# Optimization experiments

Hardware: AMD Instinct MI355X
Metric: run time of the kernel (lower is better)

## Reference

```python
import jax, jax.numpy as jnp
import numpy as np

B, S1, S2, E, P = 8, 2048, 2048, 1024, 1024


def setup_inputs() -> dict:
    key = jax.random.key(0)
    k1, k2, k3, k4, k5 = jax.random.split(key, 5)
    query = jax.random.normal(k1, (B, S1, E), dtype=jnp.float32)
    key_t = jax.random.normal(k2, (B, S2, E), dtype=jnp.float32)
    value = jax.random.normal(k3, (B, S2, E), dtype=jnp.float32)
    # nn.Linear(E, P): weight (P, E), bias (P), shared by q/k/v per the source
    bound = 1.0 / np.sqrt(E)
    W = jax.random.uniform(k4, (P, E), minval=-bound, maxval=bound, dtype=jnp.float32)
    b = jax.random.uniform(k5, (P,), minval=-bound, maxval=bound, dtype=jnp.float32)
    return {"query": query, "key": key_t, "value": value, "W": W, "b": b}


def reference(query, key, value, W, b):
    # Source applies queries_projection to all three inputs.
    q = jnp.einsum("bse,pe->bsp", query, W) + b  # (B,S1,P)
    k = jnp.einsum("bse,pe->bsp", key, W) + b    # (B,S2,P)
    v = jnp.einsum("bse,pe->bsp", value, W) + b  # (B,S2,P)
    scale = 1.0 / jnp.sqrt(jnp.float32(k.shape[-1]))
    scores = jnp.einsum("bqp,bkp->bqk", q, k) * scale  # (B,S1,S2)
    weights = jax.nn.softmax(scores, axis=-1)
    return jnp.einsum("bqk,bkp->bqp", weights, v)  # (B,S1,P)
```

## Files before the change

### kernel.cpp

```cpp
#include <hip/hip_runtime.h>


typedef unsigned short u16;
typedef __bf16 bf16x8 __attribute__((ext_vector_type(8)));
typedef float f32x4 __attribute__((ext_vector_type(4)));

__device__ __forceinline__ float b2f(u16 u) {
    union { unsigned i; float f; } x; x.i = ((unsigned)u) << 16; return x.f;
}
__device__ __forceinline__ u16 f2b(float f) {
    union { float f; unsigned i; } x; x.f = f;
    unsigned r = x.i + 0x7FFFu + ((x.i >> 16) & 1u);
    return (u16)(r >> 16);
}

__global__ __launch_bounds__(256)
void convert_f32_bf16(const float* __restrict__ src, u16* __restrict__ dst, long n)
{
    long i = ((long)blockIdx.x * 256 + threadIdx.x) * 8;
    if (i >= n) return;
    const float4* s = (const float4*)(src + i);
    float4 a = s[0], b = s[1];
    ushort4 lo, hi;
    lo.x = f2b(a.x); lo.y = f2b(a.y); lo.z = f2b(a.z); lo.w = f2b(a.w);
    hi.x = f2b(b.x); hi.y = f2b(b.y); hi.z = f2b(b.z); hi.w = f2b(b.w);
    *(ushort4*)(dst + i) = lo;
    *(ushort4*)(dst + i + 4) = hi;
}


#define BARX()   __builtin_amdgcn_s_barrier()
#define WAITL0() asm volatile("s_waitcnt lgkmcnt(0)" ::: "memory")
#define WV4()    asm volatile("s_waitcnt vmcnt(4)" ::: "memory")
#define WV0()    asm volatile("s_waitcnt vmcnt(0)" ::: "memory")
#define PRIO1()  __builtin_amdgcn_s_setprio(1)
#define PRIO0()  __builtin_amdgcn_s_setprio(0)

__global__ __launch_bounds__(512, 2)
void gemm8(const u16* __restrict__ A, const u16* __restrict__ B,
           void* __restrict__ C, const u16* __restrict__ bias,
           int K, float alpha, int em, int ldc,
           long zA, long zB, long zC, int pw, int ph)
{
    __shared__ __align__(16) u16 lds[65536];

    const int z = blockIdx.z;
    const u16* Ap = A + zA * z;
    const u16* Bp = B + zB * z;
    const long coff = zC * z;

    int tx = blockIdx.x, ty = blockIdx.y;
    if (pw > 0) {
        const int gx = gridDim.x;
        const int lin = ty * gx + tx;
        const int xcd = lin & 7, ii = lin >> 3;
        const int pcols = gx / pw;
        const int pr = xcd / pcols, pc = xcd - pr * pcols;
        tx = pc * pw + (ii % pw);
        ty = pr * ph + (ii / pw);
    }
    const int bm0 = ty << 8, bn0 = tx << 8;

    const int tid = threadIdx.x;
    const int wave = tid >> 6, lane = tid & 63;
    const int wm = wave >> 2, wn = wave & 3;
    const int quad = lane >> 4, l15 = lane & 15;
    const int sw = l15 & 7;

    const int srow = (wave << 3) + (lane >> 3);
    const int sgc  = (((lane & 7) ^ (lane >> 3)) << 3);
    const int sdst = (wave << 9) + (lane << 3);

#define STG_A(b, h, kt) do {                                                          \
    _Pragma("unroll")                                                                 \
    for (int q_ = 0; q_ < 2; ++q_)                                                    \
        __builtin_amdgcn_global_load_lds(                                             \
            (const __attribute__((address_space(1))) void*)(                          \
                Ap + (long)(bm0 + (h)*128 + q_*64 + srow) * K + (kt) + sgc),          \
            (__attribute__((address_space(3))) void*)(                                \
                lds + (b)*32768 + ((h)*128 + q_*64)*64 + sdst),                       \
            16, 0, 0);                                                                \
} while (0)

#define STG_B(b, h, kt) do {                                                          \
    _Pragma("unroll")                                                                 \
    for (int q_ = 0; q_ < 2; ++q_)                                                    \
        __builtin_amdgcn_global_load_lds(                                             \
            (const __attribute__((address_space(1))) void*)(                          \
                Bp + (long)(bn0 + (h)*128 + q_*64 + srow) * K + (kt) + sgc),          \
            (__attribute__((address_space(3))) void*)(                                \
                lds + (b)*32768 + 16384 + ((h)*128 + q_*64)*64 + sdst),               \
            16, 0, 0);                                                                \
} while (0)

#define LDA(b, m, kk) (*(const bf16x8*)(lds + (b)*32768 +                             \
    ((wm << 7) + ((m) << 4) + l15) * 64 + (((((kk) << 2) + quad) ^ sw) << 3)))
#define LDB(b, n, kk) (*(const bf16x8*)(lds + (b)*32768 + 16384 +                     \
    ((wn << 6) + ((n) << 4) + l15) * 64 + (((((kk) << 2) + quad) ^ sw) << 3)))

#define RD_A(b, mh) do {                                                              \
    _Pragma("unroll") for (int mr = 0; mr < 4; ++mr)                                  \
    _Pragma("unroll") for (int kk = 0; kk < 2; ++kk)                                  \
        af[mr][kk] = LDA(b, (mh)*4 + mr, kk);                                         \
} while (0)
#define RD_B(b, nh) do {                                                              \
    _Pragma("unroll") for (int j = 0; j < 2; ++j)                                     \
    _Pragma("unroll") for (int kk = 0; kk < 2; ++kk)                                  \
        bq[nh][j][kk] = LDB(b, (nh)*2 + j, kk);                                       \
} while (0)

#define MMAQ(mh, nh) do {                                                             \
    _Pragma("unroll") for (int mr = 0; mr < 4; ++mr)                                  \
    _Pragma("unroll") for (int j = 0; j < 2; ++j)                                     \
    _Pragma("unroll") for (int kk = 0; kk < 2; ++kk)                                  \
        acc[(mh)*4 + mr][(nh)*2 + j] = __builtin_amdgcn_mfma_f32_16x16x32_bf16(       \
            af[mr][kk], bq[nh][j][kk], acc[(mh)*4 + mr][(nh)*2 + j], 0, 0, 0);        \
} while (0)

    f32x4 acc[8][4];
#pragma unroll
    for (int m = 0; m < 8; ++m)
#pragma unroll
        for (int n = 0; n < 4; ++n) acc[m][n] = f32x4{0.f, 0.f, 0.f, 0.f};

    bf16x8 af[4][2];
    bf16x8 bq[2][2][2];

    STG_B(0, 0, 0); STG_B(0, 1, 0);
    STG_A(0, 0, 0); STG_A(0, 1, 0);
    STG_B(1, 0, 64); STG_B(1, 1, 64);
    WV4(); BARX();

    const int NI = K >> 7;
    for (int i = 0; i < NI - 1; ++i) {
        const int kt0 = i << 7;
        const int kt1 = kt0 + 64, kt2 = kt0 + 128, kt3 = kt0 + 192;
        RD_A(0, 0); RD_B(0, 0); STG_A(1, 0, kt1);
        BARX(); WAITL0(); PRIO1(); MMAQ(0, 0); PRIO0(); BARX();
        RD_B(0, 1); STG_A(1, 1, kt1);
        BARX(); WAITL0(); PRIO1(); MMAQ(0, 1); PRIO0(); BARX();
        RD_A(0, 1); STG_B(0, 0, kt2);
        BARX(); WAITL0(); PRIO1(); MMAQ(1, 0); PRIO0(); BARX();
        STG_B(0, 1, kt2);
        BARX(); PRIO1(); MMAQ(1, 1); PRIO0(); WV4(); BARX();
        RD_A(1, 0); RD_B(1, 0); STG_A(0, 0, kt2);
        BARX(); WAITL0(); PRIO1(); MMAQ(0, 0); PRIO0(); BARX();
        RD_B(1, 1); STG_A(0, 1, kt2);
        BARX(); WAITL0(); PRIO1(); MMAQ(0, 1); PRIO0(); BARX();
        RD_A(1, 1); STG_B(1, 0, kt3);
        BARX(); WAITL0(); PRIO1(); MMAQ(1, 0); PRIO0(); BARX();
        STG_B(1, 1, kt3);
        BARX(); PRIO1(); MMAQ(1, 1); PRIO0(); WV4(); BARX();
    }
    {
        const int kt1 = ((NI - 1) << 7) + 64;
        RD_A(0, 0); RD_B(0, 0); STG_A(1, 0, kt1);
        BARX(); WAITL0(); PRIO1(); MMAQ(0, 0); PRIO0(); BARX();
        RD_B(0, 1); STG_A(1, 1, kt1);
        BARX(); WAITL0(); PRIO1(); MMAQ(0, 1); PRIO0(); BARX();
        RD_A(0, 1);
        BARX(); WAITL0(); PRIO1(); MMAQ(1, 0); PRIO0(); BARX();
        PRIO1(); MMAQ(1, 1); PRIO0(); WV0(); BARX();
        RD_A(1, 0); RD_B(1, 0);
        BARX(); WAITL0(); PRIO1(); MMAQ(0, 0); PRIO0(); BARX();
        RD_B(1, 1);
        BARX(); WAITL0(); PRIO1(); MMAQ(0, 1); PRIO0(); BARX();
        RD_A(1, 1);
        BARX(); WAITL0(); PRIO1(); MMAQ(1, 0); PRIO0(); BARX();
        PRIO1(); MMAQ(1, 1); PRIO0();
    }

#pragma unroll
    for (int m = 0; m < 8; ++m) {
        const int row = bm0 + (wm << 7) + (m << 4) + (quad << 2);
#pragma unroll
        for (int n = 0; n < 4; ++n) {
            const int col = bn0 + (wn << 6) + (n << 4) + l15;
            const float bv = bias ? b2f(bias[col]) : 0.f;
            f32x4 v = acc[m][n];
            const float o0 = alpha * v[0] + bv;
            const float o1 = alpha * v[1] + bv;
            const float o2 = alpha * v[2] + bv;
            const float o3 = alpha * v[3] + bv;
            if (em == 2) {
                ushort4 pk;
                pk.x = f2b(o0); pk.y = f2b(o1); pk.z = f2b(o2); pk.w = f2b(o3);
                *(ushort4*)((u16*)C + coff + ((long)(row >> 11) << 21)
                            + ((long)col << 11) + (row & 2047)) = pk;
            } else if (em == 1) {
                float* Cf = (float*)C + coff;
                Cf[(long)(row + 0) * ldc + col] = o0;
                Cf[(long)(row + 1) * ldc + col] = o1;
                Cf[(long)(row + 2) * ldc + col] = o2;
                Cf[(long)(row + 3) * ldc + col] = o3;
            } else {
                u16* Cb = (u16*)C + coff;
                Cb[(long)(row + 0) * ldc + col] = f2b(o0);
                Cb[(long)(row + 1) * ldc + col] = f2b(o1);
                Cb[(long)(row + 2) * ldc + col] = f2b(o2);
                Cb[(long)(row + 3) * ldc + col] = f2b(o3);
            }
        }
    }
}

__global__ __launch_bounds__(256)
void softmax_rows(u16* __restrict__ S)
{
    const long row = blockIdx.x;
    u16* p = S + (row << 11);
    const int tid = threadIdx.x, wave = tid >> 6, lane = tid & 63;

    union { uint4 q; u16 u[8]; } d;
    d.q = ((const uint4*)p)[tid];
    float v[8];
#pragma unroll
    for (int i = 0; i < 8; i++) v[i] = b2f(d.u[i]);

    float m = v[0];
#pragma unroll
    for (int i = 1; i < 8; i++) m = fmaxf(m, v[i]);
#pragma unroll
    for (int o = 32; o; o >>= 1) m = fmaxf(m, __shfl_xor(m, o, 64));
    __shared__ float redm[4], reds[4];
    if (lane == 0) redm[wave] = m;
    __syncthreads();
    m = fmaxf(fmaxf(redm[0], redm[1]), fmaxf(redm[2], redm[3]));

    float e[8], s = 0.f;
#pragma unroll
    for (int i = 0; i < 8; i++) { e[i] = __expf(v[i] - m); s += e[i]; }
#pragma unroll
    for (int o = 32; o; o >>= 1) s += __shfl_xor(s, o, 64);
    if (lane == 0) reds[wave] = s;
    __syncthreads();
    s = reds[0] + reds[1] + reds[2] + reds[3];

    const float inv = 1.f / s;
#pragma unroll
    for (int i = 0; i < 8; i++) d.u[i] = f2b(e[i] * inv);
    ((uint4*)p)[tid] = d.q;
}

extern "C" void kernel_launch(void* const* d_in, const int* in_sizes, int n_in,
                              void* d_out, int out_size, void* d_ws, size_t ws_size,
                              hipStream_t stream) {
    const float* query = (const float*)d_in[0];
    const float* key   = (const float*)d_in[1];
    const float* value = (const float*)d_in[2];
    const float* W     = (const float*)d_in[3];
    const float* bias  = (const float*)d_in[4];
    float* out = (float*)d_out;

    u16* sc  = (u16*)d_ws;
    u16* xc  = (u16*)d_ws;
    u16* Wc  = (u16*)d_ws + 16777216L;
    u16* bc  = Wc + 1048576L;
    u16* qb  = (u16*)d_ws + 33554432L;
    u16* kb  = qb + 16777216L;
    u16* vT  = kb + 16777216L;

    const dim3 blk2(256), blk5(512);

    convert_f32_bf16<<<dim3(512), blk2, 0, stream>>>(W, Wc, 1048576L);
    convert_f32_bf16<<<dim3(1),   blk2, 0, stream>>>(bias, bc, 1024L);

    convert_f32_bf16<<<dim3(8192), blk2, 0, stream>>>(query, xc, 16777216L);
    gemm8<<<dim3(4, 64, 1), blk5, 0, stream>>>(xc, Wc, qb, bc,
        1024, 1.f, 0, 1024, 0, 0, 0, 4, 8);
    convert_f32_bf16<<<dim3(8192), blk2, 0, stream>>>(key, xc, 16777216L);
    gemm8<<<dim3(4, 64, 1), blk5, 0, stream>>>(xc, Wc, kb, bc,
        1024, 1.f, 0, 1024, 0, 0, 0, 4, 8);
    convert_f32_bf16<<<dim3(8192), blk2, 0, stream>>>(value, xc, 16777216L);
    gemm8<<<dim3(4, 64, 1), blk5, 0, stream>>>(xc, Wc, vT, bc,
        1024, 1.f, 2, 0, 0, 0, 0, 4, 8);

    gemm8<<<dim3(8, 8, 8), blk5, 0, stream>>>(qb, kb, sc, nullptr,
        1024, 0.03125f, 0, 2048, 2048L * 1024, 2048L * 1024, 2048L * 2048, 8, 1);

    softmax_rows<<<dim3(16384), blk2, 0, stream>>>(sc);

    gemm8<<<dim3(4, 8, 8), blk5, 0, stream>>>(sc, vT, out, nullptr,
        2048, 1.f, 1, 1024, 2048L * 2048, 1024L * 2048, 2048L * 1024, 4, 1);
}
```

Measured before the change: 490.6 us.

## Batch Q/K/V projections into one launch and remap block-to-XCD tiling

Converts query, key and value to bf16 up front into separate buffers, using the output buffer as scratch for the value copy and the weights. The three projection GEMMs then run as one grid of 768 blocks, with z selecting the input and the output mode (row-major or transposed V). The goal is to fill the GPU better and remove launch gaps between the serial 256-block projection GEMMs. It also replaces the pw/ph XCD swizzle with new block remaps: rmap 1 interleaves z across XCDs for the attention GEMMs, and rmap 2 gives each XCD a contiguous range of projection tiles. In exchange it needs more workspace and adds per-block remap arithmetic.

```diff
diff --git a/kernel.cpp b/kernel.cpp
--- a/kernel.cpp
+++ b/kernel.cpp
@@ -37,28 +37,33 @@
 #define PRIO0()  __builtin_amdgcn_s_setprio(0)
 
 __global__ __launch_bounds__(512, 2)
-void gemm8(const u16* __restrict__ A, const u16* __restrict__ B,
+void gemm8(const u16* __restrict__ A0, const u16* __restrict__ A1,
+           const u16* __restrict__ A2, const u16* __restrict__ B,
            void* __restrict__ C, const u16* __restrict__ bias,
            int K, float alpha, int em, int ldc,
-           long zA, long zB, long zC, int pw, int ph)
+           long zA, long zB, long zC, int rmap)
 {
     __shared__ __align__(16) u16 lds[65536];
 
-    const int z = blockIdx.z;
-    const u16* Ap = A + zA * z;
+    int tx = blockIdx.x, ty = blockIdx.y, z = blockIdx.z;
+    if (rmap == 1) {
+        const int gx = gridDim.x, gxy = gx * gridDim.y;
+        const int g = tx + ty * gx + z * gxy;
+        const int r = g >> 3;
+        z = g & 7; tx = r % gx; ty = r / gx;
+    } else if (rmap == 2) {
+        const int g = tx + ty * 4 + z * 256;
+        const int xcd = g & 7, i = g >> 3;
+        const int G = xcd * 24 + (i >> 2);
+        tx = i & 3; z = G >> 6; ty = G & 63;
+    }
+
+    const int eff5 = (em == 5);
+    const u16* Ap = eff5 ? (z == 0 ? A0 : (z == 1 ? A1 : A2)) : A0 + zA * z;
     const u16* Bp = B + zB * z;
     const long coff = zC * z;
-
-    int tx = blockIdx.x, ty = blockIdx.y;
-    if (pw > 0) {
-        const int gx = gridDim.x;
-        const int lin = ty * gx + tx;
-        const int xcd = lin & 7, ii = lin >> 3;
-        const int pcols = gx / pw;
-        const int pr = xcd / pcols, pc = xcd - pr * pcols;
-        tx = pc * pw + (ii % pw);
-        ty = pr * ph + (ii / pw);
-    }
+    const int eme = eff5 ? (z == 2 ? 2 : 0) : em;
+
     const int bm0 = ty << 8, bn0 = tx << 8;
 
     const int tid = threadIdx.x;
@@ -182,12 +187,12 @@
             const float o1 = alpha * v[1] + bv;
             const float o2 = alpha * v[2] + bv;
             const float o3 = alpha * v[3] + bv;
-            if (em == 2) {
+            if (eme == 2) {
                 ushort4 pk;
                 pk.x = f2b(o0); pk.y = f2b(o1); pk.z = f2b(o2); pk.w = f2b(o3);
                 *(ushort4*)((u16*)C + coff + ((long)(row >> 11) << 21)
                             + ((long)col << 11) + (row & 2047)) = pk;
-            } else if (em == 1) {
+            } else if (eme == 1) {
                 float* Cf = (float*)C + coff;
                 Cf[(long)(row + 0) * ldc + col] = o0;
                 Cf[(long)(row + 1) * ldc + col] = o1;
@@ -253,33 +258,31 @@
     float* out = (float*)d_out;
 
     u16* sc  = (u16*)d_ws;
-    u16* xc  = (u16*)d_ws;
-    u16* Wc  = (u16*)d_ws + 16777216L;
-    u16* bc  = Wc + 1048576L;
+    u16* xq  = (u16*)d_ws;
+    u16* xk  = (u16*)d_ws + 16777216L;
     u16* qb  = (u16*)d_ws + 33554432L;
     u16* kb  = qb + 16777216L;
     u16* vT  = kb + 16777216L;
+    u16* xv  = (u16*)d_out;
+    u16* Wc  = (u16*)d_out + 16777216L;
+    u16* bc  = Wc + 1048576L;
 
     const dim3 blk2(256), blk5(512);
 
-    convert_f32_bf16<<<dim3(512), blk2, 0, stream>>>(W, Wc, 1048576L);
-    convert_f32_bf16<<<dim3(1),   blk2, 0, stream>>>(bias, bc, 1024L);
-
-    convert_f32_bf16<<<dim3(8192), blk2, 0, stream>>>(query, xc, 16777216L);
-    gemm8<<<dim3(4, 64, 1), blk5, 0, stream>>>(xc, Wc, qb, bc,
-        1024, 1.f, 0, 1024, 0, 0, 0, 4, 8);
-    convert_f32_bf16<<<dim3(8192), blk2, 0, stream>>>(key, xc, 16777216L);
-    gemm8<<<dim3(4, 64, 1), blk5, 0, stream>>>(xc, Wc, kb, bc,
-        1024, 1.f, 0, 1024, 0, 0, 0, 4, 8);
-    convert_f32_bf16<<<dim3(8192), blk2, 0, stream>>>(value, xc, 16777216L);
-    gemm8<<<dim3(4, 64, 1), blk5, 0, stream>>>(xc, Wc, vT, bc,
-        1024, 1.f, 2, 0, 0, 0, 0, 4, 8);
-
-    gemm8<<<dim3(8, 8, 8), blk5, 0, stream>>>(qb, kb, sc, nullptr,
-        1024, 0.03125f, 0, 2048, 2048L * 1024, 2048L * 1024, 2048L * 2048, 8, 1);
+    convert_f32_bf16<<<dim3(512),  blk2, 0, stream>>>(W, Wc, 1048576L);
+    convert_f32_bf16<<<dim3(1),    blk2, 0, stream>>>(bias, bc, 1024L);
+    convert_f32_bf16<<<dim3(8192), blk2, 0, stream>>>(query, xq, 16777216L);
+    convert_f32_bf16<<<dim3(8192), blk2, 0, stream>>>(key,   xk, 16777216L);
+    convert_f32_bf16<<<dim3(8192), blk2, 0, stream>>>(value, xv, 16777216L);
+
+    gemm8<<<dim3(4, 64, 3), blk5, 0, stream>>>(xq, xk, xv, Wc, qb, bc,
+        1024, 1.f, 5, 1024, 0, 0, 16777216L, 2);
+
+    gemm8<<<dim3(8, 8, 8), blk5, 0, stream>>>(qb, nullptr, nullptr, kb, sc, nullptr,
+        1024, 0.03125f, 0, 2048, 2048L * 1024, 2048L * 1024, 2048L * 2048, 1);
 
     softmax_rows<<<dim3(16384), blk2, 0, stream>>>(sc);
 
-    gemm8<<<dim3(4, 8, 8), blk5, 0, stream>>>(sc, vT, out, nullptr,
-        2048, 1.f, 1, 1024, 2048L * 2048, 1024L * 2048, 2048L * 1024, 4, 1);
-}
+    gemm8<<<dim3(4, 8, 8), blk5, 0, stream>>>(sc, nullptr, nullptr, vT, out, nullptr,
+        2048, 1.f, 1, 1024, 2048L * 2048, 1024L * 2048, 2048L * 1024, 1);
+}
```

Measured after the change: 498.2 us. About the same (+1.5%).
